# Optimization experiments

Measured on AMD Instinct MI355X. Metric: run time of the kernel, lower is better.

The kernel has to match this reference:

```python
import jax, jax.numpy as jnp
import numpy as np

K = 20
EPS = 1e-5
NEG_SLOPE = 0.2


def knn_idx(x, k):
    # x: [B, C, N]; returns indices of k nearest neighbors [B, N, k]
    xx = jnp.sum(x * x, axis=1)                      # [B, N]
    inner = jnp.einsum('bcn,bcm->bnm', x, x)         # [B, N, N]
    neg_dist = 2.0 * inner - xx[:, :, None] - xx[:, None, :]
    return jax.lax.top_k(neg_dist, k)[1]             # [B, N, k]


def graph_feature(x, k):
    # x: [B, C, N] -> [B, 2C, N, k]
    idx = knn_idx(x, k)
    xT = jnp.transpose(x, (0, 2, 1))                 # [B, N, C]
    nbrs = jax.vmap(lambda feats, ids: feats[ids])(xT, idx)   # [B, N, k, C]
    ctr = jnp.broadcast_to(xT[:, :, None, :], nbrs.shape)
    feat = jnp.concatenate([nbrs - ctr, ctr], axis=-1)        # [B, N, k, 2C]
    return jnp.transpose(feat, (0, 3, 1, 2))


def bn(x, g, b, axes):
    # training-mode batchnorm over `axes`, channel dim = 1
    m = jnp.mean(x, axis=axes, keepdims=True)
    v = jnp.var(x, axis=axes, keepdims=True)
    shape = [1] * x.ndim
    shape[1] = -1
    g = g.reshape(shape)
    b = b.reshape(shape)
    return g * (x - m) * jax.lax.rsqrt(v + EPS) + b


def lrelu(x):
    return jax.nn.leaky_relu(x, NEG_SLOPE)


def setup_inputs() -> dict:
    key = jax.random.key(0)
    ks = jax.random.split(key, 4)
    x = jax.random.normal(ks[0], (4, 16, 512, 3), dtype=jnp.float32)
    w1 = jax.random.normal(ks[1], (64, 6), dtype=jnp.float32) * 0.1
    w2 = jax.random.normal(ks[2], (256, 128), dtype=jnp.float32) * 0.05
    w3 = jax.random.normal(ks[3], (512, 320), dtype=jnp.float32) * 0.05
    ones = jnp.ones
    zeros = jnp.zeros
    return {
        'x': x,
        'w1': w1, 'g1': ones(64, jnp.float32), 'b1': zeros(64, jnp.float32),
        'w2': w2, 'g2': ones(256, jnp.float32), 'b2': zeros(256, jnp.float32),
        'w3': w3, 'g3': ones(512, jnp.float32), 'b3': zeros(512, jnp.float32),
    }


def reference(x, w1, g1, b1, w2, g2, b2, w3, g3, b3):
    B, P, N, D = x.shape
    xp = jnp.transpose(x.reshape(B * P, N, D), (0, 2, 1))    # [BP, 3, N]

    f = graph_feature(xp, K)                                  # [BP, 6, N, K]
    h = lrelu(bn(jnp.einsum('bcnk,oc->bonk', f, w1), g1, b1, (0, 2, 3)))
    x1 = jnp.max(h, axis=-1)                                  # [BP, 64, N]

    f = graph_feature(x1, K)                                  # [BP, 128, N, K]
    h = lrelu(bn(jnp.einsum('bcnk,oc->bonk', f, w2), g2, b2, (0, 2, 3)))
    x2 = jnp.max(h, axis=-1)                                  # [BP, 256, N]

    cat = jnp.concatenate([x1, x2], axis=1)                   # [BP, 320, N]
    h = lrelu(bn(jnp.einsum('bcn,oc->bon', cat, w3), g3, b3, (0, 2)))  # [BP, 512, N]

    pooled = jnp.concatenate([jnp.max(h, axis=-1), jnp.mean(h, axis=-1)], axis=1)  # [BP, 1024]
    return pooled.reshape(B, P, -1)
```

## Files before the change

kernel.cpp:

```cpp
#include <hip/hip_runtime.h>
#include <hip/hip_bf16.h>
#include <math.h>

#define NBP 64
#define NP  512
#define KK  20

using short8 = __attribute__((ext_vector_type(8))) short;
using f32x4  = __attribute__((ext_vector_type(4))) float;

constexpr size_t O_X1   = 0;
constexpr size_t O_XCH  = 8388608;
constexpr size_t O_XCL  = 29360128;
constexpr size_t O_D    = 50331648;
constexpr size_t O_IDX  = 117440512;
constexpr size_t O_XX2  = 120061952;
constexpr size_t O_WC   = 120193024;
constexpr size_t O_W3H  = 120324096;
constexpr size_t O_W3L  = 120651776;
constexpr size_t O_SC1  = 120979456;
constexpr size_t O_SC2  = 120979968;
constexpr size_t O_SC3  = 120982016;
constexpr size_t O_ST1  = 120986112;
constexpr size_t O_ST2  = 120994304;
constexpr size_t O_ST3  = 121125376;
constexpr size_t STATS_BYTES = 8192 + 131072 + 262144;

__global__ __launch_bounds__(256) void prepw_kernel(const float* __restrict__ w2,
                                                    const float* __restrict__ w3,
                                                    float* __restrict__ Wcat,
                                                    __hip_bfloat16* __restrict__ w3h,
                                                    __hip_bfloat16* __restrict__ w3l) {
    int i = blockIdx.x * 256 + threadIdx.x;
    if (i < 32768) {
        int c = i >> 9, q = i & 511;
        Wcat[i] = (q < 256) ? w2[q * 128 + c]
                            : (w2[(q - 256) * 128 + 64 + c] - w2[(q - 256) * 128 + c]);
    } else if (i < 32768 + 163840) {
        int j = i - 32768;
        float v = w3[j];
        __hip_bfloat16 h = __float2bfloat16(v);
        w3h[j] = h;
        w3l[j] = __float2bfloat16(v - __bfloat162float(h));
    }
}

__device__ __forceinline__ void wave_top20_set(const float v[8], int lane, int* __restrict__ outp) {
    unsigned u[8];
#pragma unroll
    for (int q = 0; q < 8; q++) {
        unsigned b = __float_as_uint(v[q]);
        u[q] = (b & 0x80000000u) ? ~b : (b | 0x80000000u);
    }
    unsigned T = 0u;
    for (int b = 31; b >= 0; b--) {
        unsigned cand = T | (1u << b);
        int cnt = 0;
#pragma unroll
        for (int q = 0; q < 8; q++)
            cnt += __popcll(__ballot(u[q] >= cand));
        if (cnt >= KK) T = cand;
    }
    unsigned long long lmask = (1ull << lane) - 1ull;
    int slotbase = 0;
#pragma unroll
    for (int q = 0; q < 8; q++) {
        unsigned long long bgt = __ballot(u[q] > T);
        if (u[q] > T) {
            int slot = slotbase + __popcll(bgt & lmask);
            outp[slot] = lane + (q << 6);
        }
        slotbase += __popcll(bgt);
    }
    int need = KK - slotbase;
#pragma unroll
    for (int q = 0; q < 8; q++) {
        if (need > 0) {
            unsigned long long beq = __ballot(u[q] == T);
            int cq = __popcll(beq);
            int take = need < cq ? need : cq;
            if (u[q] == T) {
                int p = __popcll(beq & lmask);
                if (p < take) outp[slotbase + p] = lane + (q << 6);
            }
            slotbase += take;
            need -= take;
        }
    }
}

__global__ __launch_bounds__(256) void knn1_kernel(const float* __restrict__ x, int* __restrict__ idx1) {
    __shared__ float px[NP * 3];
    __shared__ float sxx[NP];
    int bp = blockIdx.x >> 7;
    int pg = blockIdx.x & 127;
    int wid = threadIdx.x >> 6;
    int lane = threadIdx.x & 63;
    int n = pg * 4 + wid;
    const float* xb = x + (size_t)bp * NP * 3;
    for (int i = threadIdx.x; i < NP * 3; i += 256) px[i] = xb[i];
    __syncthreads();
    for (int i = threadIdx.x; i < NP; i += 256) {
        float a = px[i * 3], b = px[i * 3 + 1], c = px[i * 3 + 2];
        sxx[i] = a * a + b * b + c * c;
    }
    __syncthreads();
    float rn0 = px[n * 3], rn1 = px[n * 3 + 1], rn2 = px[n * 3 + 2];
    float xxn = sxx[n];
    float v[8];
#pragma unroll
    for (int q = 0; q < 8; q++) {
        int m = lane + (q << 6);
        float dot = rn0 * px[m * 3] + rn1 * px[m * 3 + 1] + rn2 * px[m * 3 + 2];
        v[q] = 2.0f * dot - xxn - sxx[m];
    }
    wave_top20_set(v, lane, idx1 + ((size_t)bp * NP + n) * KK);
}

__global__ __launch_bounds__(256) void conv1_kernel(const float* __restrict__ x, const float* __restrict__ w1,
                                                    const int* __restrict__ idx1,
                                                    float* __restrict__ h1max, float* __restrict__ h1min,
                                                    double* __restrict__ stats1) {
    __shared__ double red1[4][64][2];
    int bp = blockIdx.x >> 5;
    int nt = blockIdx.x & 31;
    int n0 = nt * 16;
    int o  = threadIdx.x & 63;
    int nq = threadIdx.x >> 6;
    const float* xb = x + (size_t)bp * NP * 3;
    float w[6];
#pragma unroll
    for (int c = 0; c < 6; c++) w[c] = w1[o * 6 + c];
    double s = 0.0, s2 = 0.0;
    float omx[4], omn[4];
#pragma unroll
    for (int nn = 0; nn < 4; nn++) {
        int n = n0 + nq * 4 + nn;
        float c0 = xb[n * 3], c1 = xb[n * 3 + 1], c2 = xb[n * 3 + 2];
        const int* ip = idx1 + ((size_t)bp * NP + n) * KK;
        float mx = -INFINITY, mn = INFINITY;
        for (int k = 0; k < KK; k++) {
            int j = ip[k];
            float e0 = xb[j * 3], e1 = xb[j * 3 + 1], e2 = xb[j * 3 + 2];
            float h = w[0] * (e0 - c0) + w[1] * (e1 - c1) + w[2] * (e2 - c2)
                    + w[3] * c0 + w[4] * c1 + w[5] * c2;
            mx = fmaxf(mx, h); mn = fminf(mn, h);
            s += (double)h; s2 += (double)h * (double)h;
        }
        omx[nn] = mx; omn[nn] = mn;
    }
    size_t base = ((size_t)bp * 64 + o) * NP + n0 + nq * 4;
    *(float4*)&h1max[base] = make_float4(omx[0], omx[1], omx[2], omx[3]);
    *(float4*)&h1min[base] = make_float4(omn[0], omn[1], omn[2], omn[3]);
    red1[nq][o][0] = s; red1[nq][o][1] = s2;
    __syncthreads();
    if (threadIdx.x < 64) {
        int oo = threadIdx.x;
        double S = 0, S2 = 0;
        for (int q = 0; q < 4; q++) { S += red1[q][oo][0]; S2 += red1[q][oo][1]; }
        int copy = blockIdx.x & 7;
        atomicAdd(&stats1[(copy * 64 + oo) * 2], S);
        atomicAdd(&stats1[(copy * 64 + oo) * 2 + 1], S2);
    }
}

__global__ __launch_bounds__(256) void fprep_kernel(const double* __restrict__ stats, int ncopy, int nch,
                                                    double invN, const float* __restrict__ g,
                                                    const float* __restrict__ b, float* __restrict__ scsh) {
    int o = blockIdx.x * 256 + threadIdx.x;
    if (o >= nch) return;
    double S = 0, S2 = 0;
    for (int c = 0; c < ncopy; c++) {
        S  += stats[((size_t)c * nch + o) * 2];
        S2 += stats[((size_t)c * nch + o) * 2 + 1];
    }
    double m = S * invN;
    double v = S2 * invN - m * m;
    double sc = (double)g[o] / sqrt(v + 1e-5);
    scsh[o * 2]     = (float)sc;
    scsh[o * 2 + 1] = (float)((double)b[o] - sc * m);
}

__global__ __launch_bounds__(256) void fin1_kernel(const float* __restrict__ h1max, const float* __restrict__ h1min,
                                                   const float* __restrict__ scsh,
                                                   float* __restrict__ x1,
                                                   __hip_bfloat16* __restrict__ XCh,
                                                   __hip_bfloat16* __restrict__ XCl) {
    __shared__ float tile[64][33];
    int bp = blockIdx.x >> 4, nt = blockIdx.x & 15, n0 = nt * 32;
    for (int i = threadIdx.x; i < 64 * 32; i += 256) {
        int o = i >> 5, nl = i & 31;
        float sc = scsh[o * 2], sh = scsh[o * 2 + 1];
        size_t gi = ((size_t)bp * 64 + o) * NP + n0 + nl;
        float v = (sc >= 0.0f) ? h1max[gi] : h1min[gi];
        float y = sc * v + sh;
        y = (y >= 0.0f) ? y : 0.2f * y;
        x1[gi] = y;
        tile[o][nl] = y;
    }
    __syncthreads();
    for (int i = threadIdx.x; i < 64 * 32; i += 256) {
        int nl = i >> 6, o = i & 63;
        float y = tile[o][nl];
        __hip_bfloat16 h = __float2bfloat16(y);
        size_t base = ((size_t)bp * NP + n0 + nl) * 320 + o;
        XCh[base] = h;
        XCl[base] = __float2bfloat16(y - __bfloat162float(h));
    }
}

__global__ __launch_bounds__(256) void xx2_kernel(const float* __restrict__ x1, float* __restrict__ xx2v) {
    int i = blockIdx.x * 256 + threadIdx.x;
    int bp = i >> 9, n = i & 511;
    const float* xb = x1 + (size_t)bp * 64 * NP + n;
    float acc = 0.0f;
    for (int c = 0; c < 64; c++) { float v = xb[c * NP]; acc += v * v; }
    xx2v[i] = acc;
}

__global__ __launch_bounds__(256) void gram_kernel(const float* __restrict__ x1, const float* __restrict__ xx2v,
                                                   float* __restrict__ Dm) {
    __shared__ float An[64 * 128];
    __shared__ float Bm[64 * 128];
    int bp = blockIdx.x >> 4;
    int ntb = (blockIdx.x >> 2) & 3, mtb = blockIdx.x & 3;
    int n0 = ntb * 128, m0 = mtb * 128;
    const float* xb = x1 + (size_t)bp * 64 * NP;
    for (int i = threadIdx.x; i < 64 * 128; i += 256) {
        int c = i >> 7, r = i & 127;
        An[i] = xb[c * NP + n0 + r];
        Bm[i] = xb[c * NP + m0 + r];
    }
    __syncthreads();
    int ng = threadIdx.x & 15, mg = threadIdx.x >> 4;
    float acc[8][8];
#pragma unroll
    for (int r = 0; r < 8; r++)
#pragma unroll
        for (int j = 0; j < 8; j++) acc[r][j] = 0.0f;
    const float* ap = An + ng * 8;
    const float* bq = Bm + mg * 8;
#pragma unroll 2
    for (int c = 0; c < 64; c++) {
        float4 a0 = *(const float4*)(ap + c * 128);
        float4 a1 = *(const float4*)(ap + c * 128 + 4);
        float4 b0 = *(const float4*)(bq + c * 128);
        float4 b1 = *(const float4*)(bq + c * 128 + 4);
        float av[8] = {a0.x, a0.y, a0.z, a0.w, a1.x, a1.y, a1.z, a1.w};
        float bv[8] = {b0.x, b0.y, b0.z, b0.w, b1.x, b1.y, b1.z, b1.w};
#pragma unroll
        for (int r = 0; r < 8; r++)
#pragma unroll
            for (int j = 0; j < 8; j++) acc[r][j] += av[r] * bv[j];
    }
    float xm[8];
#pragma unroll
    for (int j = 0; j < 8; j++) xm[j] = xx2v[bp * NP + m0 + mg * 8 + j];
#pragma unroll
    for (int r = 0; r < 8; r++) {
        float xxn = xx2v[bp * NP + n0 + ng * 8 + r];
        float out[8];
#pragma unroll
        for (int j = 0; j < 8; j++) out[j] = 2.0f * acc[r][j] - xxn - xm[j];
        size_t base = ((size_t)bp * NP + n0 + ng * 8 + r) * NP + m0 + mg * 8;
        *(float4*)&Dm[base]     = make_float4(out[0], out[1], out[2], out[3]);
        *(float4*)&Dm[base + 4] = make_float4(out[4], out[5], out[6], out[7]);
    }
}

__global__ __launch_bounds__(256) void topk2_kernel(const float* __restrict__ Dm, int* __restrict__ idx2) {
    int wid = threadIdx.x >> 6;
    int lane = threadIdx.x & 63;
    int row = blockIdx.x * 4 + wid;
    const float* dr = Dm + (size_t)row * NP;
    float v[8];
#pragma unroll
    for (int q = 0; q < 8; q++) v[q] = dr[lane + (q << 6)];
    wave_top20_set(v, lane, idx2 + (size_t)row * KK);
}

__global__ __launch_bounds__(256) void conv2a_kernel(const float* __restrict__ x1, const float* __restrict__ Wcat,
                                                     float* __restrict__ Aout, float* __restrict__ Dtout) {
    __shared__ float An[64 * 128];
    __shared__ float Bm[64 * 128];
    int bp = blockIdx.x >> 4;
    int ntb = (blockIdx.x >> 2) & 3, qtb = blockIdx.x & 3;
    int n0 = ntb * 128, q0 = qtb * 128;
    const float* xb = x1 + (size_t)bp * 64 * NP;
    for (int i = threadIdx.x; i < 64 * 128; i += 256) {
        int c = i >> 7, r = i & 127;
        An[i] = xb[c * NP + n0 + r];
        Bm[i] = Wcat[c * 512 + q0 + r];
    }
    __syncthreads();
    int ng = threadIdx.x & 15, mg = threadIdx.x >> 4;
    float acc[8][8];
#pragma unroll
    for (int r = 0; r < 8; r++)
#pragma unroll
        for (int j = 0; j < 8; j++) acc[r][j] = 0.0f;
    const float* ap = An + ng * 8;
    const float* bq = Bm + mg * 8;
#pragma unroll 2
    for (int c = 0; c < 64; c++) {
        float4 a0 = *(const float4*)(ap + c * 128);
        float4 a1 = *(const float4*)(ap + c * 128 + 4);
        float4 b0 = *(const float4*)(bq + c * 128);
        float4 b1 = *(const float4*)(bq + c * 128 + 4);
        float av[8] = {a0.x, a0.y, a0.z, a0.w, a1.x, a1.y, a1.z, a1.w};
        float bv[8] = {b0.x, b0.y, b0.z, b0.w, b1.x, b1.y, b1.z, b1.w};
#pragma unroll
        for (int r = 0; r < 8; r++)
#pragma unroll
            for (int j = 0; j < 8; j++) acc[r][j] += av[r] * bv[j];
    }
    float* ob = (q0 < 256) ? Aout : Dtout;
    int qoff = (q0 & 255) + mg * 8;
#pragma unroll
    for (int r = 0; r < 8; r++) {
        size_t base = ((size_t)bp * NP + n0 + ng * 8 + r) * 256 + qoff;
        *(float4*)&ob[base]     = make_float4(acc[r][0], acc[r][1], acc[r][2], acc[r][3]);
        *(float4*)&ob[base + 4] = make_float4(acc[r][4], acc[r][5], acc[r][6], acc[r][7]);
    }
}

__global__ __launch_bounds__(256) void conv2b_kernel(const float* __restrict__ A, const float* __restrict__ Dt,
                                                     const int* __restrict__ idx2,
                                                     double* __restrict__ stats2) {
    __shared__ float Al[512 * 16];
    __shared__ double red[16][16][2];
    int bid = blockIdx.x;
    int bp = bid >> 5;
    int ot = (bid >> 1) & 15, nh = bid & 1;
    int o0 = ot * 16, n0 = nh * 256;
    int tid = threadIdx.x;
    for (int i = tid; i < 2048; i += 256) {
        int j = i >> 2, p = i & 3;
        *(float4*)&Al[j * 16 + p * 4] = *(const float4*)&A[((size_t)bp * NP + j) * 256 + o0 + p * 4];
    }
    __syncthreads();
    int o = tid & 15, np = tid >> 4;
    double sh = 0.0, sh2 = 0.0;
    for (int nn = 0; nn < 16; nn++) {
        int n = n0 + np * 16 + nn;
        const int* ip = idx2 + ((size_t)bp * NP + n) * KK;
        int4 ia = *(const int4*)ip, ib = *(const int4*)(ip + 4), ic = *(const int4*)(ip + 8);
        int4 id4 = *(const int4*)(ip + 12), ie = *(const int4*)(ip + 16);
        int js[20] = {ia.x, ia.y, ia.z, ia.w, ib.x, ib.y, ib.z, ib.w, ic.x, ic.y, ic.z, ic.w,
                      id4.x, id4.y, id4.z, id4.w, ie.x, ie.y, ie.z, ie.w};
        float dv = Dt[((size_t)bp * NP + n) * 256 + o0 + o];
        float s1 = 0.0f, s2 = 0.0f;
#pragma unroll
        for (int k = 0; k < KK; k++) {
            float a = Al[js[k] * 16 + o];
            s1 += a; s2 += a * a;
        }
        sh  += (double)s1 + 20.0 * (double)dv;
        sh2 += (double)s2 + 2.0 * (double)dv * (double)s1 + 20.0 * (double)dv * (double)dv;
    }
    red[np][o][0] = sh; red[np][o][1] = sh2;
    __syncthreads();
    if (tid < 16) {
        double S = 0, S2 = 0;
        for (int q = 0; q < 16; q++) { S += red[q][tid][0]; S2 += red[q][tid][1]; }
        int copy = bid & 31;
        atomicAdd(&stats2[(copy * 256 + o0 + tid) * 2], S);
        atomicAdd(&stats2[(copy * 256 + o0 + tid) * 2 + 1], S2);
    }
}

__global__ __launch_bounds__(256) void fin2g_kernel(const float* __restrict__ A, const float* __restrict__ Dt,
                                                    const int* __restrict__ idx2,
                                                    const float* __restrict__ scsh,
                                                    __hip_bfloat16* __restrict__ XCh,
                                                    __hip_bfloat16* __restrict__ XCl) {
    __shared__ float Al[512 * 16];
    int bid = blockIdx.x;
    int bp = bid >> 5;
    int ot = (bid >> 1) & 15, nh = bid & 1;
    int o0 = ot * 16, n0 = nh * 256;
    int tid = threadIdx.x;
    for (int i = tid; i < 2048; i += 256) {
        int j = i >> 2, p = i & 3;
        *(float4*)&Al[j * 16 + p * 4] = *(const float4*)&A[((size_t)bp * NP + j) * 256 + o0 + p * 4];
    }
    __syncthreads();
    int o = tid & 15, np = tid >> 4;
    float sc = scsh[(o0 + o) * 2], shift = scsh[(o0 + o) * 2 + 1];
    for (int nn = 0; nn < 16; nn++) {
        int n = n0 + np * 16 + nn;
        const int* ip = idx2 + ((size_t)bp * NP + n) * KK;
        int4 ia = *(const int4*)ip, ib = *(const int4*)(ip + 4), ic = *(const int4*)(ip + 8);
        int4 id4 = *(const int4*)(ip + 12), ie = *(const int4*)(ip + 16);
        int js[20] = {ia.x, ia.y, ia.z, ia.w, ib.x, ib.y, ib.z, ib.w, ic.x, ic.y, ic.z, ic.w,
                      id4.x, id4.y, id4.z, id4.w, ie.x, ie.y, ie.z, ie.w};
        float dv = Dt[((size_t)bp * NP + n) * 256 + o0 + o];
        float mx = -INFINITY, mn = INFINITY;
#pragma unroll
        for (int k = 0; k < KK; k++) {
            float a = Al[js[k] * 16 + o];
            mx = fmaxf(mx, a); mn = fminf(mn, a);
        }
        float v = ((sc >= 0.0f) ? mx : mn) + dv;
        float y = sc * v + shift;
        y = (y >= 0.0f) ? y : 0.2f * y;
        __hip_bfloat16 h = __float2bfloat16(y);
        size_t base = ((size_t)bp * NP + n) * 320 + 64 + o0 + o;
        XCh[base] = h;
        XCl[base] = __float2bfloat16(y - __bfloat162float(h));
    }
}

__global__ __launch_bounds__(256) void conv3m_kernel(const __hip_bfloat16* __restrict__ XCh,
                                                     const __hip_bfloat16* __restrict__ XCl,
                                                     const __hip_bfloat16* __restrict__ w3h,
                                                     const __hip_bfloat16* __restrict__ w3l,
                                                     float* __restrict__ h3,
                                                     double* __restrict__ stats3) {
    __shared__ __align__(16) char smem[4 * 64 * 40 * 2];
    __hip_bfloat16* Wh = (__hip_bfloat16*)smem;
    __hip_bfloat16* Wl = Wh + 64 * 40;
    __hip_bfloat16* Xh = Wl + 64 * 40;
    __hip_bfloat16* Xl = Xh + 64 * 40;
    int bid = blockIdx.x;
    int bp = bid >> 6, ot = (bid >> 3) & 7, nt = bid & 7;
    int o0 = ot * 64, n0 = nt * 64;
    int tid = threadIdx.x, l = tid & 63, w = tid >> 6;
    int wo = (w >> 1) * 32, wn = (w & 1) * 32;
    int sr = tid >> 2, sq = tid & 3;
    int lrow = l & 15, lk = (l >> 4) * 8;
    f32x4 z4 = {0.f, 0.f, 0.f, 0.f};
    f32x4 acc[2][2] = {{z4, z4}, {z4, z4}};
    for (int ct = 0; ct < 10; ct++) {
        int c0 = ct * 32;
        __syncthreads();
        *(float4*)(Wh + sr * 40 + sq * 8) = *(const float4*)(w3h + (size_t)(o0 + sr) * 320 + c0 + sq * 8);
        *(float4*)(Wl + sr * 40 + sq * 8) = *(const float4*)(w3l + (size_t)(o0 + sr) * 320 + c0 + sq * 8);
        *(float4*)(Xh + sr * 40 + sq * 8) = *(const float4*)(XCh + ((size_t)bp * NP + n0 + sr) * 320 + c0 + sq * 8);
        *(float4*)(Xl + sr * 40 + sq * 8) = *(const float4*)(XCl + ((size_t)bp * NP + n0 + sr) * 320 + c0 + sq * 8);
        __syncthreads();
        short8 ah[2], al[2], bh[2], bl[2];
#pragma unroll
        for (int t = 0; t < 2; t++) {
            ah[t] = *(const short8*)(Wh + (wo + t * 16 + lrow) * 40 + lk);
            al[t] = *(const short8*)(Wl + (wo + t * 16 + lrow) * 40 + lk);
            bh[t] = *(const short8*)(Xh + (wn + t * 16 + lrow) * 40 + lk);
            bl[t] = *(const short8*)(Xl + (wn + t * 16 + lrow) * 40 + lk);
        }
#pragma unroll
        for (int mt = 0; mt < 2; mt++)
#pragma unroll
            for (int nl2 = 0; nl2 < 2; nl2++) {
                acc[mt][nl2] = __builtin_amdgcn_mfma_f32_16x16x32_bf16(al[mt], bh[nl2], acc[mt][nl2], 0, 0, 0);
                acc[mt][nl2] = __builtin_amdgcn_mfma_f32_16x16x32_bf16(ah[mt], bl[nl2], acc[mt][nl2], 0, 0, 0);
                acc[mt][nl2] = __builtin_amdgcn_mfma_f32_16x16x32_bf16(ah[mt], bh[nl2], acc[mt][nl2], 0, 0, 0);
            }
    }
    __syncthreads();
    double* redD = (double*)smem;
    size_t hb = (size_t)bp * 512;
#pragma unroll
    for (int mt = 0; mt < 2; mt++) {
#pragma unroll
        for (int rg = 0; rg < 4; rg++) {
            int og = o0 + wo + mt * 16 + (l >> 4) * 4 + rg;
            double s = 0.0, s2 = 0.0;
#pragma unroll
            for (int nl2 = 0; nl2 < 2; nl2++) {
                float h = acc[mt][nl2][rg];
                int ng = n0 + wn + nl2 * 16 + (l & 15);
                h3[(hb + og) * 512 + ng] = h;
                s += (double)h; s2 += (double)h * (double)h;
            }
#pragma unroll
            for (int off = 1; off < 16; off <<= 1) {
                s  += __shfl_xor(s, off);
                s2 += __shfl_xor(s2, off);
            }
            if ((l & 15) == 0) {
                int ol = wo + mt * 16 + (l >> 4) * 4 + rg;
                redD[((w & 1) * 64 + ol) * 2]     = s;
                redD[((w & 1) * 64 + ol) * 2 + 1] = s2;
            }
        }
    }
    __syncthreads();
    if (tid < 64) {
        double S  = redD[tid * 2]     + redD[(64 + tid) * 2];
        double S2 = redD[tid * 2 + 1] + redD[(64 + tid) * 2 + 1];
        int copy = bid & 31;
        atomicAdd(&stats3[(copy * 512 + o0 + tid) * 2], S);
        atomicAdd(&stats3[(copy * 512 + o0 + tid) * 2 + 1], S2);
    }
}

__global__ __launch_bounds__(256) void pool_kernel(const float* __restrict__ h3, const float* __restrict__ scsh3,
                                                   float* __restrict__ out) {
    int row = blockIdx.x * 4 + (threadIdx.x >> 6);
    int lane = threadIdx.x & 63;
    int bp = row >> 9, o = row & 511;
    float sc = scsh3[o * 2], sh = scsh3[o * 2 + 1];
    const float* hr = h3 + (size_t)row * NP;
    float4 v0 = *(const float4*)&hr[lane * 4];
    float4 v1 = *(const float4*)&hr[256 + lane * 4];
    float vs[8] = {v0.x, v0.y, v0.z, v0.w, v1.x, v1.y, v1.z, v1.w};
    float mx = -INFINITY, sm = 0.0f;
#pragma unroll
    for (int q = 0; q < 8; q++) {
        float y = sc * vs[q] + sh;
        y = (y >= 0.0f) ? y : 0.2f * y;
        mx = fmaxf(mx, y); sm += y;
    }
    for (int off = 32; off >= 1; off >>= 1) {
        mx = fmaxf(mx, __shfl_xor(mx, off));
        sm += __shfl_xor(sm, off);
    }
    if (lane == 0) {
        out[(size_t)bp * 1024 + o]       = mx;
        out[(size_t)bp * 1024 + 512 + o] = sm * (1.0f / 512.0f);
    }
}

extern "C" void kernel_launch(void* const* d_in, const int* in_sizes, int n_in,
                              void* d_out, int out_size, void* d_ws, size_t ws_size,
                              hipStream_t stream) {
    const float* x  = (const float*)d_in[0];
    const float* w1 = (const float*)d_in[1];
    const float* g1 = (const float*)d_in[2];
    const float* b1 = (const float*)d_in[3];
    const float* w2 = (const float*)d_in[4];
    const float* g2 = (const float*)d_in[5];
    const float* b2 = (const float*)d_in[6];
    const float* w3 = (const float*)d_in[7];
    const float* g3 = (const float*)d_in[8];
    const float* b3 = (const float*)d_in[9];
    float* out = (float*)d_out;
    char* ws = (char*)d_ws;

    float*          x1    = (float*)(ws + O_X1);
    __hip_bfloat16* XCh   = (__hip_bfloat16*)(ws + O_XCH);
    __hip_bfloat16* XCl   = (__hip_bfloat16*)(ws + O_XCL);
    float*          Dbuf  = (float*)(ws + O_D);
    int*            idx   = (int*)(ws + O_IDX);
    float*          xx2v  = (float*)(ws + O_XX2);
    float*          Wcat  = (float*)(ws + O_WC);
    __hip_bfloat16* w3h   = (__hip_bfloat16*)(ws + O_W3H);
    __hip_bfloat16* w3l   = (__hip_bfloat16*)(ws + O_W3L);
    float*          scsh1 = (float*)(ws + O_SC1);
    float*          scsh2 = (float*)(ws + O_SC2);
    float*          scsh3 = (float*)(ws + O_SC3);
    double*         st1   = (double*)(ws + O_ST1);
    double*         st2   = (double*)(ws + O_ST2);
    double*         st3   = (double*)(ws + O_ST3);

    float* h1max = Dbuf;
    float* h1min = Dbuf + 2097152;
    float* Abuf  = Dbuf;
    float* Dt    = Dbuf + 8388608;
    float* h3    = Dbuf;

    hipMemsetAsync(ws + O_ST1, 0, STATS_BYTES, stream);
    prepw_kernel<<<768, 256, 0, stream>>>(w2, w3, Wcat, w3h, w3l);
    knn1_kernel<<<8192, 256, 0, stream>>>(x, idx);
    conv1_kernel<<<2048, 256, 0, stream>>>(x, w1, idx, h1max, h1min, st1);
    fprep_kernel<<<1, 256, 0, stream>>>(st1, 8, 64, 1.0 / 655360.0, g1, b1, scsh1);
    fin1_kernel<<<1024, 256, 0, stream>>>(h1max, h1min, scsh1, x1, XCh, XCl);
    xx2_kernel<<<128, 256, 0, stream>>>(x1, xx2v);
    gram_kernel<<<1024, 256, 0, stream>>>(x1, xx2v, Dbuf);
    topk2_kernel<<<8192, 256, 0, stream>>>(Dbuf, idx);
    conv2a_kernel<<<1024, 256, 0, stream>>>(x1, Wcat, Abuf, Dt);
    conv2b_kernel<<<2048, 256, 0, stream>>>(Abuf, Dt, idx, st2);
    fprep_kernel<<<1, 256, 0, stream>>>(st2, 32, 256, 1.0 / 655360.0, g2, b2, scsh2);
    fin2g_kernel<<<2048, 256, 0, stream>>>(Abuf, Dt, idx, scsh2, XCh, XCl);
    conv3m_kernel<<<4096, 256, 0, stream>>>(XCh, XCl, w3h, w3l, h3, st3);
    fprep_kernel<<<2, 256, 0, stream>>>(st3, 32, 512, 1.0 / 32768.0, g3, b3, scsh3);
    pool_kernel<<<8192, 256, 0, stream>>>(h3, scsh3, out);
}
```

Baseline: 474.4 us.

## Enlarge conv3 GEMM tile to 128x64 with K=64 steps and XOR-swizzled LDS

The conv3 split-bf16 GEMM kernel now computes a 128-output by 64-point tile per block with a K step of 64, where before it used a 64x64 tile with a K step of 32. This halves the block count and the number of sync barriers, and each loaded tile is reused across more MFMAs. The shared-memory layout moves from padded rows to an XOR swizzle to avoid bank conflicts, and all global loads are issued into registers before being stored to LDS. The cost is more registers per thread (accumulators and 12 staged float4s) and larger LDS, which may reduce occupancy.

```diff
diff --git a/kernel.cpp b/kernel.cpp
--- a/kernel.cpp
+++ b/kernel.cpp
@@ -417,59 +417,80 @@
                                                      const __hip_bfloat16* __restrict__ w3l,
                                                      float* __restrict__ h3,
                                                      double* __restrict__ stats3) {
-    __shared__ __align__(16) char smem[4 * 64 * 40 * 2];
-    __hip_bfloat16* Wh = (__hip_bfloat16*)smem;
-    __hip_bfloat16* Wl = Wh + 64 * 40;
-    __hip_bfloat16* Xh = Wl + 64 * 40;
-    __hip_bfloat16* Xl = Xh + 64 * 40;
+    __shared__ __align__(16) __hip_bfloat16 smem3[384 * 64];
     int bid = blockIdx.x;
-    int bp = bid >> 6, ot = (bid >> 3) & 7, nt = bid & 7;
-    int o0 = ot * 64, n0 = nt * 64;
+    int bp = bid >> 5, ot = (bid >> 3) & 3, nt = bid & 7;
+    int o0 = ot * 128, n0 = nt * 64;
     int tid = threadIdx.x, l = tid & 63, w = tid >> 6;
-    int wo = (w >> 1) * 32, wn = (w & 1) * 32;
-    int sr = tid >> 2, sq = tid & 3;
-    int lrow = l & 15, lk = (l >> 4) * 8;
+    int wo = (w >> 1) * 64, wn = (w & 1) * 32;
+    int lrow = l & 15, lj = l >> 4;
     f32x4 z4 = {0.f, 0.f, 0.f, 0.f};
-    f32x4 acc[2][2] = {{z4, z4}, {z4, z4}};
-    for (int ct = 0; ct < 10; ct++) {
-        int c0 = ct * 32;
+    f32x4 acc[4][2];
+#pragma unroll
+    for (int mt = 0; mt < 4; mt++) { acc[mt][0] = z4; acc[mt][1] = z4; }
+    for (int ct = 0; ct < 5; ct++) {
+        int c0 = ct * 64;
         __syncthreads();
-        *(float4*)(Wh + sr * 40 + sq * 8) = *(const float4*)(w3h + (size_t)(o0 + sr) * 320 + c0 + sq * 8);
-        *(float4*)(Wl + sr * 40 + sq * 8) = *(const float4*)(w3l + (size_t)(o0 + sr) * 320 + c0 + sq * 8);
-        *(float4*)(Xh + sr * 40 + sq * 8) = *(const float4*)(XCh + ((size_t)bp * NP + n0 + sr) * 320 + c0 + sq * 8);
-        *(float4*)(Xl + sr * 40 + sq * 8) = *(const float4*)(XCl + ((size_t)bp * NP + n0 + sr) * 320 + c0 + sq * 8);
+        float4 vals[12];
+#pragma unroll
+        for (int t = 0; t < 12; t++) {
+            int i = tid + t * 256;
+            int row = i >> 3, ch = i & 7;
+            const __hip_bfloat16* src;
+            if (row < 128)      src = w3h + (size_t)(o0 + row) * 320;
+            else if (row < 256) src = w3l + (size_t)(o0 + row - 128) * 320;
+            else if (row < 320) src = XCh + ((size_t)bp * NP + n0 + row - 256) * 320;
+            else                src = XCl + ((size_t)bp * NP + n0 + row - 320) * 320;
+            vals[t] = *(const float4*)(src + c0 + ch * 8);
+        }
+#pragma unroll
+        for (int t = 0; t < 12; t++) {
+            int i = tid + t * 256;
+            int row = i >> 3, ch = i & 7;
+            *(float4*)(smem3 + row * 64 + ((ch ^ (row & 7)) * 8)) = vals[t];
+        }
         __syncthreads();
-        short8 ah[2], al[2], bh[2], bl[2];
-#pragma unroll
-        for (int t = 0; t < 2; t++) {
-            ah[t] = *(const short8*)(Wh + (wo + t * 16 + lrow) * 40 + lk);
-            al[t] = *(const short8*)(Wl + (wo + t * 16 + lrow) * 40 + lk);
-            bh[t] = *(const short8*)(Xh + (wn + t * 16 + lrow) * 40 + lk);
-            bl[t] = *(const short8*)(Xl + (wn + t * 16 + lrow) * 40 + lk);
-        }
-#pragma unroll
-        for (int mt = 0; mt < 2; mt++)
-#pragma unroll
-            for (int nl2 = 0; nl2 < 2; nl2++) {
-                acc[mt][nl2] = __builtin_amdgcn_mfma_f32_16x16x32_bf16(al[mt], bh[nl2], acc[mt][nl2], 0, 0, 0);
-                acc[mt][nl2] = __builtin_amdgcn_mfma_f32_16x16x32_bf16(ah[mt], bl[nl2], acc[mt][nl2], 0, 0, 0);
-                acc[mt][nl2] = __builtin_amdgcn_mfma_f32_16x16x32_bf16(ah[mt], bh[nl2], acc[mt][nl2], 0, 0, 0);
+#pragma unroll
+        for (int ks = 0; ks < 2; ks++) {
+            short8 ah[4], al[4], bh[2], bl[2];
+#pragma unroll
+            for (int t = 0; t < 4; t++) {
+                int r = wo + t * 16 + lrow;
+                int c = (lj + 4 * ks) ^ (r & 7);
+                ah[t] = *(const short8*)(smem3 + r * 64 + c * 8);
+                al[t] = *(const short8*)(smem3 + (128 + r) * 64 + c * 8);
             }
-    }
-    __syncthreads();
-    double* redD = (double*)smem;
+#pragma unroll
+            for (int t = 0; t < 2; t++) {
+                int r = wn + t * 16 + lrow;
+                int c = (lj + 4 * ks) ^ (r & 7);
+                bh[t] = *(const short8*)(smem3 + (256 + r) * 64 + c * 8);
+                bl[t] = *(const short8*)(smem3 + (320 + r) * 64 + c * 8);
+            }
+#pragma unroll
+            for (int mt = 0; mt < 4; mt++)
+#pragma unroll
+                for (int nl = 0; nl < 2; nl++) {
+                    acc[mt][nl] = __builtin_amdgcn_mfma_f32_16x16x32_bf16(al[mt], bh[nl], acc[mt][nl], 0, 0, 0);
+                    acc[mt][nl] = __builtin_amdgcn_mfma_f32_16x16x32_bf16(ah[mt], bl[nl], acc[mt][nl], 0, 0, 0);
+                    acc[mt][nl] = __builtin_amdgcn_mfma_f32_16x16x32_bf16(ah[mt], bh[nl], acc[mt][nl], 0, 0, 0);
+                }
+        }
+    }
+    __syncthreads();
+    double* redD = (double*)smem3;
     size_t hb = (size_t)bp * 512;
 #pragma unroll
-    for (int mt = 0; mt < 2; mt++) {
+    for (int mt = 0; mt < 4; mt++) {
 #pragma unroll
         for (int rg = 0; rg < 4; rg++) {
-            int og = o0 + wo + mt * 16 + (l >> 4) * 4 + rg;
+            int ol = wo + mt * 16 + lj * 4 + rg;
             double s = 0.0, s2 = 0.0;
 #pragma unroll
-            for (int nl2 = 0; nl2 < 2; nl2++) {
-                float h = acc[mt][nl2][rg];
-                int ng = n0 + wn + nl2 * 16 + (l & 15);
-                h3[(hb + og) * 512 + ng] = h;
+            for (int nl = 0; nl < 2; nl++) {
+                float h = acc[mt][nl][rg];
+                int ng = n0 + wn + nl * 16 + lrow;
+                h3[(hb + o0 + ol) * 512 + ng] = h;
                 s += (double)h; s2 += (double)h * (double)h;
             }
 #pragma unroll
@@ -477,17 +498,16 @@
                 s  += __shfl_xor(s, off);
                 s2 += __shfl_xor(s2, off);
             }
-            if ((l & 15) == 0) {
-                int ol = wo + mt * 16 + (l >> 4) * 4 + rg;
-                redD[((w & 1) * 64 + ol) * 2]     = s;
-                redD[((w & 1) * 64 + ol) * 2 + 1] = s2;
+            if (lrow == 0) {
+                redD[((w & 1) * 128 + ol) * 2]     = s;
+                redD[((w & 1) * 128 + ol) * 2 + 1] = s2;
             }
         }
     }
     __syncthreads();
-    if (tid < 64) {
-        double S  = redD[tid * 2]     + redD[(64 + tid) * 2];
-        double S2 = redD[tid * 2 + 1] + redD[(64 + tid) * 2 + 1];
+    if (tid < 128) {
+        double S  = redD[tid * 2]     + redD[(128 + tid) * 2];
+        double S2 = redD[tid * 2 + 1] + redD[(128 + tid) * 2 + 1];
         int copy = bid & 31;
         atomicAdd(&stats3[(copy * 512 + o0 + tid) * 2], S);
         atomicAdd(&stats3[(copy * 512 + o0 + tid) * 2 + 1], S2);
@@ -572,7 +592,7 @@
     conv2b_kernel<<<2048, 256, 0, stream>>>(Abuf, Dt, idx, st2);
     fprep_kernel<<<1, 256, 0, stream>>>(st2, 32, 256, 1.0 / 655360.0, g2, b2, scsh2);
     fin2g_kernel<<<2048, 256, 0, stream>>>(Abuf, Dt, idx, scsh2, XCh, XCl);
-    conv3m_kernel<<<4096, 256, 0, stream>>>(XCh, XCl, w3h, w3l, h3, st3);
+    conv3m_kernel<<<2048, 256, 0, stream>>>(XCh, XCl, w3h, w3l, h3, st3);
     fprep_kernel<<<2, 256, 0, stream>>>(st3, 32, 512, 1.0 / 32768.0, g3, b3, scsh3);
     pool_kernel<<<8192, 256, 0, stream>>>(h3, scsh3, out);
 }
```

After: 466.6 us. Within noise of the previous version (-1.7%).
